# Performance work log

Measured on AMD Instinct MI355X. Metric: run time of the kernel, lower is better.

The kernel has to match this reference:

```python
import jax, jax.numpy as jnp
import numpy as np

ROWS, COLS, H, W = 128, 128, 128, 128
B, C = 2, 16
DENSITY = 0.01  # classic Hough vote matrix is very sparse binary


def setup_inputs() -> dict:
    key = jax.random.key(0)
    k_img, k_vote = jax.random.split(key)
    image = jax.random.normal(k_img, (B, C, ROWS, COLS), dtype=jnp.float32)
    # sparse binary voting matrix, shape (rows, cols, h, w)
    vote_index = (jax.random.uniform(k_vote, (ROWS, COLS, H, W)) < DENSITY).astype(jnp.float32)
    return {"image": image, "vote_index": vote_index}


def reference(image, vote_index):
    rows, cols, h, w = vote_index.shape
    b, c = image.shape[0], image.shape[1]
    V = vote_index.reshape(rows * cols, h * w)          # (rows*cols, h*w)
    x = jax.nn.relu(image.reshape(b * c, rows * cols))  # (b*c, rows*cols)
    ht = (x @ V) / cols                                 # (b*c, h*w)
    return ht.reshape(b, c, h, w)
```

## Files before the change

### kernel.cpp

```cpp
#include <hip/hip_runtime.h>

constexpr int Mdim = 32;
constexpr int Kdim = 16384;
constexpr int Ndim = 16384;

constexpr int TPB = 256;

constexpr int NB      = 128;
constexpr int NTILES  = Ndim / NB;
constexpr int KT      = 8;
constexpr int KC      = Kdim / KT;
constexpr int KB      = 64;
constexpr int NCHUNK  = KC / KB;
constexpr int LROW    = 132;

typedef short bf16x8 __attribute__((ext_vector_type(8)));
typedef float f32x4  __attribute__((ext_vector_type(4)));

__device__ __forceinline__ short f32_to_bf16(float f) {
    union { float f; unsigned u; } c; c.f = f;
    unsigned u = c.u;
    u += 0x7fffu + ((u >> 16) & 1u);
    return (short)(u >> 16);
}

__global__ __launch_bounds__(TPB)
void build_xa(const float* __restrict__ image, short* __restrict__ xa) {
    const int g    = blockIdx.x * TPB + threadIdx.x;
    const int lane = g & 63;
    const int frag = g >> 6;
    const int mt   = frag & 1;
    const int kc   = frag >> 1;
    const int m    = mt * 16 + (lane & 15);
    const int k    = kc * 32 + (lane >> 4) * 8;
    const float* src = image + (size_t)m * Kdim + k;

    bf16x8 o;
    #pragma unroll
    for (int j = 0; j < 8; ++j)
        o[j] = f32_to_bf16(fmaxf(src[j], 0.0f) * (1.0f / 128.0f));
    reinterpret_cast<bf16x8*>(xa)[g] = o;
}

__global__ __launch_bounds__(TPB)
void ht_gemm(const short* __restrict__ xa,
             const float* __restrict__ vote,
             float* __restrict__ parts)
{
    __shared__ short lds[2][KB * LROW];

    const int tid    = threadIdx.x;
    const int lane   = tid & 63;
    const int w      = tid >> 6;
    const int ntile  = blockIdx.x & (NTILES - 1);
    const int kchunk = blockIdx.x >> 7;
    const int k0     = kchunk * KC;
    const int n0     = ntile * NB;

    const int s_k  = tid >> 5;
    const int s_c4 = tid & 31;

    const int bq = lane >> 4;
    const int bn = lane & 15;

    f32x4 acc[2][2];
    #pragma unroll
    for (int a = 0; a < 2; ++a)
        #pragma unroll
        for (int b = 0; b < 2; ++b) { f32x4 z = {0.f, 0.f, 0.f, 0.f}; acc[a][b] = z; }

    float4 tmp[8];

    auto load_tile = [&](int ch) {
        const float* s = vote + ((size_t)(k0 + ch * KB + s_k)) * Ndim + n0 + s_c4 * 4;
        #pragma unroll
        for (int i = 0; i < 8; ++i)
            tmp[i] = *reinterpret_cast<const float4*>(s + (size_t)(i * 8) * Ndim);
    };
    auto write_tile = [&](int buf) {
        #pragma unroll
        for (int i = 0; i < 8; ++i) {
            const int kk    = i * 8 + s_k;
            const int colsw = ((s_c4 * 4) + (((kk >> 3) & 3) << 4)) & 127;
            *reinterpret_cast<short4*>(&lds[buf][kk * LROW + colsw]) =
                make_short4(f32_to_bf16(tmp[i].x), f32_to_bf16(tmp[i].y),
                            f32_to_bf16(tmp[i].z), f32_to_bf16(tmp[i].w));
        }
    };
    auto compute = [&](int buf, int ch) {
        #pragma unroll
        for (int rs = 0; rs < KB / 32; ++rs) {
            const int kcg = (k0 >> 5) + ch * (KB / 32) + rs;
            const bf16x8 a0 = *reinterpret_cast<const bf16x8*>(
                xa + ((size_t)(kcg * 2 + 0) * 64 + lane) * 8);
            const bf16x8 a1 = *reinterpret_cast<const bf16x8*>(
                xa + ((size_t)(kcg * 2 + 1) * 64 + lane) * 8);
            #pragma unroll
            for (int cl = 0; cl < 2; ++cl) {
                const int col   = w * 32 + cl * 16 + bn;
                const int colsw = (col + (bq << 4)) & 127;
                const short* p  = &lds[buf][(rs * 32 + bq * 8) * LROW + colsw];
                bf16x8 bf;
                #pragma unroll
                for (int j = 0; j < 8; ++j) bf[j] = p[j * LROW];
                acc[0][cl] = __builtin_amdgcn_mfma_f32_16x16x32_bf16(a0, bf, acc[0][cl], 0, 0, 0);
                acc[1][cl] = __builtin_amdgcn_mfma_f32_16x16x32_bf16(a1, bf, acc[1][cl], 0, 0, 0);
            }
        }
    };

    load_tile(0);
    write_tile(0);
    for (int ch = 0; ch < NCHUNK; ++ch) {
        __syncthreads();
        if (ch + 1 < NCHUNK) load_tile(ch + 1);
        compute(ch & 1, ch);
        if (ch + 1 < NCHUNK) write_tile((ch + 1) & 1);
    }

    float* pb = parts + (size_t)kchunk * ((size_t)Mdim * Ndim);
    #pragma unroll
    for (int mt = 0; mt < 2; ++mt)
        #pragma unroll
        for (int cl = 0; cl < 2; ++cl)
            #pragma unroll
            for (int r = 0; r < 4; ++r) {
                const int row = mt * 16 + bq * 4 + r;
                const int col = n0 + w * 32 + cl * 16 + bn;
                pb[(size_t)row * Ndim + col] = acc[mt][cl][r];
            }
}

__global__ __launch_bounds__(TPB)
void ht_reduce(const float* __restrict__ parts, float* __restrict__ out, int nchunks) {
    const size_t i4 = (size_t)blockIdx.x * TPB + threadIdx.x;
    const float4* p = reinterpret_cast<const float4*>(parts) + i4;
    float4 s = make_float4(0.f, 0.f, 0.f, 0.f);
    constexpr size_t stride4 = (size_t)Mdim * Ndim / 4;
    for (int c = 0; c < nchunks; ++c) {
        const float4 v = p[(size_t)c * stride4];
        s.x += v.x; s.y += v.y; s.z += v.z; s.w += v.w;
    }
    reinterpret_cast<float4*>(out)[i4] = s;
}

__global__ __launch_bounds__(TPB)
void ht_gemm_atomic(const float* __restrict__ image, const float* __restrict__ vote,
                    float* __restrict__ out) {
    __shared__ float xsh[256 * Mdim];
    const int tid = threadIdx.x;
    const int ntile = blockIdx.x % 16;
    const int k0 = (blockIdx.x / 16) * 256;
    const int nn0 = ntile * 1024 + tid * 4;
    for (int idx = tid; idx < 256 * Mdim; idx += TPB) {
        const int kk = idx >> 5, m = idx & 31;
        xsh[idx] = fmaxf(image[(size_t)m * Kdim + (k0 + kk)], 0.0f) * (1.0f / 128.0f);
    }
    __syncthreads();
    float4 acc[Mdim];
    #pragma unroll
    for (int m = 0; m < Mdim; ++m) acc[m] = make_float4(0.f, 0.f, 0.f, 0.f);
    const float* vptr = vote + (size_t)k0 * Ndim + nn0;
    for (int kk = 0; kk < 256; ++kk) {
        const float4 v = *reinterpret_cast<const float4*>(vptr);
        vptr += Ndim;
        #pragma unroll
        for (int m = 0; m < Mdim; ++m) {
            const float s = xsh[kk * Mdim + m];
            acc[m].x = fmaf(s, v.x, acc[m].x); acc[m].y = fmaf(s, v.y, acc[m].y);
            acc[m].z = fmaf(s, v.z, acc[m].z); acc[m].w = fmaf(s, v.w, acc[m].w);
        }
    }
    #pragma unroll
    for (int m = 0; m < Mdim; ++m) {
        float* o = out + (size_t)m * Ndim + nn0;
        unsafeAtomicAdd(o + 0, acc[m].x); unsafeAtomicAdd(o + 1, acc[m].y);
        unsafeAtomicAdd(o + 2, acc[m].z); unsafeAtomicAdd(o + 3, acc[m].w);
    }
}

extern "C" void kernel_launch(void* const* d_in, const int* in_sizes, int n_in,
                              void* d_out, int out_size, void* d_ws, size_t ws_size,
                              hipStream_t stream) {
    const float* image = (const float*)d_in[0];
    const float* vote  = (const float*)d_in[1];
    float* out = (float*)d_out;

    const size_t xa_bytes    = (size_t)(Kdim / 32) * 2 * 64 * 8 * sizeof(short);
    const size_t chunk_bytes = (size_t)Mdim * Ndim * sizeof(float);

    if (xa_bytes + (size_t)KT * chunk_bytes > ws_size) {
        (void)hipMemsetAsync(out, 0, (size_t)out_size * sizeof(float), stream);
        ht_gemm_atomic<<<dim3(16 * 64), TPB, 0, stream>>>(image, vote, out);
        return;
    }

    short* xa    = (short*)d_ws;
    float* parts = (float*)((char*)d_ws + xa_bytes);

    build_xa<<<dim3((Kdim / 32) * 2 * 64 / TPB), TPB, 0, stream>>>(image, xa);
    ht_gemm<<<dim3(NTILES * KT), TPB, 0, stream>>>(xa, vote, parts);
    ht_reduce<<<dim3((Mdim * Ndim) / (4 * TPB)), TPB, 0, stream>>>(parts, out, KT);
}
```

Before: 1.329 ms.

## Transpose LDS tile with XOR swizzle and deepen register prefetch pipeline

The shared-memory tile of the vote matrix becomes n-major with an XOR swizzle, so each MFMA B-fragment is one 16-byte LDS read instead of eight strided scalar reads. Global loads are now prefetched two chunks ahead into two register slots, with one lgkmcnt-wait barrier per iteration. The K split drops from 8 to 4, which halves the partial-sum traffic and the reduction work but launches fewer blocks. The extra register buffers and the 2-block launch bound add register pressure, and the runtime-indexed tmp slot could spill to scratch if the loop is not unrolled.

```diff
diff --git a/kernel.cpp b/kernel.cpp
--- a/kernel.cpp
+++ b/kernel.cpp
@@ -8,11 +8,10 @@
 
 constexpr int NB      = 128;
 constexpr int NTILES  = Ndim / NB;
-constexpr int KT      = 8;
+constexpr int KT      = 4;
 constexpr int KC      = Kdim / KT;
 constexpr int KB      = 64;
 constexpr int NCHUNK  = KC / KB;
-constexpr int LROW    = 132;
 
 typedef short bf16x8 __attribute__((ext_vector_type(8)));
 typedef float f32x4  __attribute__((ext_vector_type(4)));
@@ -22,6 +21,13 @@
     unsigned u = c.u;
     u += 0x7fffu + ((u >> 16) & 1u);
     return (short)(u >> 16);
+}
+
+#define LDS_BARRIER() asm volatile("s_waitcnt lgkmcnt(0)\n\ts_barrier" ::: "memory")
+
+__device__ __forceinline__ int lds_addr(int n, int u) {
+    const int s = (n ^ (n >> 3)) & 7;
+    return n * 64 + ((u ^ s) & 7) * 8;
 }
 
 __global__ __launch_bounds__(TPB)
@@ -42,12 +48,12 @@
     reinterpret_cast<bf16x8*>(xa)[g] = o;
 }
 
-__global__ __launch_bounds__(TPB)
+__global__ __launch_bounds__(TPB, 2)
 void ht_gemm(const short* __restrict__ xa,
              const float* __restrict__ vote,
              float* __restrict__ parts)
 {
-    __shared__ short lds[2][KB * LROW];
+    __shared__ __align__(16) short lds[2][NB * KB];
 
     const int tid    = threadIdx.x;
     const int lane   = tid & 63;
@@ -69,53 +75,54 @@
         #pragma unroll
         for (int b = 0; b < 2; ++b) { f32x4 z = {0.f, 0.f, 0.f, 0.f}; acc[a][b] = z; }
 
-    float4 tmp[8];
-
-    auto load_tile = [&](int ch) {
-        const float* s = vote + ((size_t)(k0 + ch * KB + s_k)) * Ndim + n0 + s_c4 * 4;
+    float4 tmp[2][8];
+
+    auto load_tile = [&](int slot, int ch) {
+        const float* s = vote + ((size_t)(k0 + ch * KB + s_k * 8)) * Ndim + n0 + s_c4 * 4;
         #pragma unroll
         for (int i = 0; i < 8; ++i)
-            tmp[i] = *reinterpret_cast<const float4*>(s + (size_t)(i * 8) * Ndim);
+            tmp[slot][i] = *reinterpret_cast<const float4*>(s + (size_t)i * Ndim);
     };
-    auto write_tile = [&](int buf) {
-        #pragma unroll
-        for (int i = 0; i < 8; ++i) {
-            const int kk    = i * 8 + s_k;
-            const int colsw = ((s_c4 * 4) + (((kk >> 3) & 3) << 4)) & 127;
-            *reinterpret_cast<short4*>(&lds[buf][kk * LROW + colsw]) =
-                make_short4(f32_to_bf16(tmp[i].x), f32_to_bf16(tmp[i].y),
-                            f32_to_bf16(tmp[i].z), f32_to_bf16(tmp[i].w));
+    auto write_tile = [&](int buf, int slot) {
+        #pragma unroll
+        for (int c = 0; c < 4; ++c) {
+            const int n = s_c4 * 4 + c;
+            bf16x8 v;
+            #pragma unroll
+            for (int i = 0; i < 8; ++i) {
+                const float4 t = tmp[slot][i];
+                v[i] = f32_to_bf16(c == 0 ? t.x : c == 1 ? t.y : c == 2 ? t.z : t.w);
+            }
+            *reinterpret_cast<bf16x8*>(&lds[buf][lds_addr(n, s_k)]) = v;
         }
     };
     auto compute = [&](int buf, int ch) {
         #pragma unroll
-        for (int rs = 0; rs < KB / 32; ++rs) {
-            const int kcg = (k0 >> 5) + ch * (KB / 32) + rs;
+        for (int rs = 0; rs < 2; ++rs) {
+            const int kcg = (k0 >> 5) + ch * 2 + rs;
             const bf16x8 a0 = *reinterpret_cast<const bf16x8*>(
                 xa + ((size_t)(kcg * 2 + 0) * 64 + lane) * 8);
             const bf16x8 a1 = *reinterpret_cast<const bf16x8*>(
                 xa + ((size_t)(kcg * 2 + 1) * 64 + lane) * 8);
             #pragma unroll
             for (int cl = 0; cl < 2; ++cl) {
-                const int col   = w * 32 + cl * 16 + bn;
-                const int colsw = (col + (bq << 4)) & 127;
-                const short* p  = &lds[buf][(rs * 32 + bq * 8) * LROW + colsw];
-                bf16x8 bf;
-                #pragma unroll
-                for (int j = 0; j < 8; ++j) bf[j] = p[j * LROW];
+                const int n = w * 32 + cl * 16 + bn;
+                const bf16x8 bf = *reinterpret_cast<const bf16x8*>(
+                    &lds[buf][lds_addr(n, rs * 4 + bq)]);
                 acc[0][cl] = __builtin_amdgcn_mfma_f32_16x16x32_bf16(a0, bf, acc[0][cl], 0, 0, 0);
                 acc[1][cl] = __builtin_amdgcn_mfma_f32_16x16x32_bf16(a1, bf, acc[1][cl], 0, 0, 0);
             }
         }
     };
 
-    load_tile(0);
-    write_tile(0);
+    load_tile(0, 0);
+    load_tile(1, 1);
     for (int ch = 0; ch < NCHUNK; ++ch) {
-        __syncthreads();
-        if (ch + 1 < NCHUNK) load_tile(ch + 1);
-        compute(ch & 1, ch);
-        if (ch + 1 < NCHUNK) write_tile((ch + 1) & 1);
+        const int slot = ch & 1;
+        write_tile(slot, slot);
+        if (ch + 2 < NCHUNK) load_tile(slot, ch + 2);
+        LDS_BARRIER();
+        compute(slot, ch);
     }
 
     float* pb = parts + (size_t)kchunk * ((size_t)Mdim * Ndim);
```

Result: slower. 1.528 ms (+15.0%).

## Load vote operand directly into registers per wave, dropping LDS staging

Applied to the files above, without the earlier changes.

The GEMM kernel no longer stages the fp32 vote tile through shared memory. Each wave owns a 32-column slice and loads the B fragment straight from global memory into registers, with double-buffered register prefetch, then converts to bf16 in-register before the MFMAs. Removing the LDS round trip and block barriers cuts LDS traffic and sync stalls, and raises occupancy through launch bounds. The cost is that global loads become scalar fp32 reads strided across rows (16 per lane per slab), which may coalesce worse than the previous float4 tile loads.

```diff
diff --git a/kernel.cpp b/kernel.cpp
--- a/kernel.cpp
+++ b/kernel.cpp
@@ -6,13 +6,12 @@
 
 constexpr int TPB = 256;
 
-constexpr int NB      = 128;
-constexpr int NTILES  = Ndim / NB;
-constexpr int KT      = 8;
-constexpr int KC      = Kdim / KT;
-constexpr int KB      = 64;
-constexpr int NCHUNK  = KC / KB;
-constexpr int LROW    = 132;
+constexpr int KT     = 8;
+constexpr int KC     = Kdim / KT;
+constexpr int SLABS  = KC / 32;
+constexpr int NT32   = Ndim / 32;
+constexpr int NWAVES = NT32 * KT;
+constexpr int NBLK   = NWAVES / 4;
 
 typedef short bf16x8 __attribute__((ext_vector_type(8)));
 typedef float f32x4  __attribute__((ext_vector_type(4)));
@@ -42,26 +41,22 @@
     reinterpret_cast<bf16x8*>(xa)[g] = o;
 }
 
-__global__ __launch_bounds__(TPB)
+__global__ __launch_bounds__(TPB, 4)
 void ht_gemm(const short* __restrict__ xa,
              const float* __restrict__ vote,
              float* __restrict__ parts)
 {
-    __shared__ short lds[2][KB * LROW];
+    const int tid  = threadIdx.x;
+    const int lane = tid & 63;
+    const int w    = tid >> 6;
+    const int wv   = blockIdx.x * 4 + w;
+    const int nt   = wv & (NT32 - 1);
+    const int kch  = wv >> 9;
+    const int k0   = kch * KC;
 
-    const int tid    = threadIdx.x;
-    const int lane   = tid & 63;
-    const int w      = tid >> 6;
-    const int ntile  = blockIdx.x & (NTILES - 1);
-    const int kchunk = blockIdx.x >> 7;
-    const int k0     = kchunk * KC;
-    const int n0     = ntile * NB;
-
-    const int s_k  = tid >> 5;
-    const int s_c4 = tid & 31;
-
-    const int bq = lane >> 4;
-    const int bn = lane & 15;
+    const int bq   = lane >> 4;
+    const int bn   = lane & 15;
+    const int ncol = nt * 32 + bn;
 
     f32x4 acc[2][2];
     #pragma unroll
@@ -69,56 +64,43 @@
         #pragma unroll
         for (int b = 0; b < 2; ++b) { f32x4 z = {0.f, 0.f, 0.f, 0.f}; acc[a][b] = z; }
 
-    float4 tmp[8];
+    const float* vbase = vote + (size_t)(k0 + bq * 8) * Ndim + ncol;
+    const short* abase = xa + ((size_t)(k0 >> 5) * 128 + lane) * 8;
 
-    auto load_tile = [&](int ch) {
-        const float* s = vote + ((size_t)(k0 + ch * KB + s_k)) * Ndim + n0 + s_c4 * 4;
+    float b0[16], b1[16];
+
+    auto load_b = [&](float* d, int s) {
+        const float* p = vbase + (size_t)s * 32 * Ndim;
         #pragma unroll
-        for (int i = 0; i < 8; ++i)
-            tmp[i] = *reinterpret_cast<const float4*>(s + (size_t)(i * 8) * Ndim);
-    };
-    auto write_tile = [&](int buf) {
-        #pragma unroll
-        for (int i = 0; i < 8; ++i) {
-            const int kk    = i * 8 + s_k;
-            const int colsw = ((s_c4 * 4) + (((kk >> 3) & 3) << 4)) & 127;
-            *reinterpret_cast<short4*>(&lds[buf][kk * LROW + colsw]) =
-                make_short4(f32_to_bf16(tmp[i].x), f32_to_bf16(tmp[i].y),
-                            f32_to_bf16(tmp[i].z), f32_to_bf16(tmp[i].w));
+        for (int j = 0; j < 8; ++j) {
+            d[j]     = p[(size_t)j * Ndim];
+            d[8 + j] = p[(size_t)j * Ndim + 16];
         }
     };
-    auto compute = [&](int buf, int ch) {
+    auto compute = [&](const float* b, int s) {
+        const bf16x8 a0 = *reinterpret_cast<const bf16x8*>(abase + (size_t)s * 1024);
+        const bf16x8 a1 = *reinterpret_cast<const bf16x8*>(abase + (size_t)s * 1024 + 512);
+        bf16x8 f0, f1;
         #pragma unroll
-        for (int rs = 0; rs < KB / 32; ++rs) {
-            const int kcg = (k0 >> 5) + ch * (KB / 32) + rs;
-            const bf16x8 a0 = *reinterpret_cast<const bf16x8*>(
-                xa + ((size_t)(kcg * 2 + 0) * 64 + lane) * 8);
-            const bf16x8 a1 = *reinterpret_cast<const bf16x8*>(
-                xa + ((size_t)(kcg * 2 + 1) * 64 + lane) * 8);
-            #pragma unroll
-            for (int cl = 0; cl < 2; ++cl) {
-                const int col   = w * 32 + cl * 16 + bn;
-                const int colsw = (col + (bq << 4)) & 127;
-                const short* p  = &lds[buf][(rs * 32 + bq * 8) * LROW + colsw];
-                bf16x8 bf;
-                #pragma unroll
-                for (int j = 0; j < 8; ++j) bf[j] = p[j * LROW];
-                acc[0][cl] = __builtin_amdgcn_mfma_f32_16x16x32_bf16(a0, bf, acc[0][cl], 0, 0, 0);
-                acc[1][cl] = __builtin_amdgcn_mfma_f32_16x16x32_bf16(a1, bf, acc[1][cl], 0, 0, 0);
-            }
+        for (int j = 0; j < 8; ++j) {
+            f0[j] = f32_to_bf16(b[j]);
+            f1[j] = f32_to_bf16(b[8 + j]);
         }
+        acc[0][0] = __builtin_amdgcn_mfma_f32_16x16x32_bf16(a0, f0, acc[0][0], 0, 0, 0);
+        acc[1][0] = __builtin_amdgcn_mfma_f32_16x16x32_bf16(a1, f0, acc[1][0], 0, 0, 0);
+        acc[0][1] = __builtin_amdgcn_mfma_f32_16x16x32_bf16(a0, f1, acc[0][1], 0, 0, 0);
+        acc[1][1] = __builtin_amdgcn_mfma_f32_16x16x32_bf16(a1, f1, acc[1][1], 0, 0, 0);
     };
 
-    load_tile(0);
-    write_tile(0);
-    for (int ch = 0; ch < NCHUNK; ++ch) {
-        __syncthreads();
-        if (ch + 1 < NCHUNK) load_tile(ch + 1);
-        compute(ch & 1, ch);
-        if (ch + 1 < NCHUNK) write_tile((ch + 1) & 1);
+    load_b(b0, 0);
+    for (int s = 0; s < SLABS; s += 2) {
+        load_b(b1, s + 1);
+        compute(b0, s);
+        if (s + 2 < SLABS) load_b(b0, s + 2);
+        compute(b1, s + 1);
     }
 
-    float* pb = parts + (size_t)kchunk * ((size_t)Mdim * Ndim);
+    float* pb = parts + (size_t)kch * ((size_t)Mdim * Ndim);
     #pragma unroll
     for (int mt = 0; mt < 2; ++mt)
         #pragma unroll
@@ -126,7 +108,7 @@
             #pragma unroll
             for (int r = 0; r < 4; ++r) {
                 const int row = mt * 16 + bq * 4 + r;
-                const int col = n0 + w * 32 + cl * 16 + bn;
+                const int col = nt * 32 + cl * 16 + bn;
                 pb[(size_t)row * Ndim + col] = acc[mt][cl][r];
             }
 }
@@ -199,6 +181,6 @@
     float* parts = (float*)((char*)d_ws + xa_bytes);
 
     build_xa<<<dim3((Kdim / 32) * 2 * 64 / TPB), TPB, 0, stream>>>(image, xa);
-    ht_gemm<<<dim3(NTILES * KT), TPB, 0, stream>>>(xa, vote, parts);
+    ht_gemm<<<dim3(NBLK), TPB, 0, stream>>>(xa, vote, parts);
     ht_reduce<<<dim3((Mdim * Ndim) / (4 * TPB)), TPB, 0, stream>>>(parts, out, KT);
 }
```

New measurement: 1.328 ms. About the same (-0.1%).
